# Kernel optimization log

Hardware: AMD Instinct MI355X
Metric: run time of the kernel (lower is better)

Reference implementation:

```python
import jax, jax.numpy as jnp
import numpy as np

N_NODES = 100000
N_EDGES = 1600000
N_GRAPHS = 256
DIMS = [128, 128, 128, 128]  # gcn_layers_dim -> 3 GCNConv layers


def setup_inputs() -> dict:
    key = jax.random.key(0)
    ks = jax.random.split(key, 12)
    inp = {
        "x": jax.random.normal(ks[0], (N_NODES, DIMS[0]), jnp.float32),
        "edge_index": jax.random.randint(ks[1], (2, N_EDGES), 0, N_NODES),
        "edge_weight": jax.random.uniform(ks[2], (N_EDGES,), jnp.float32),
        "batch": jnp.sort(jax.random.randint(ks[3], (N_NODES,), 0, N_GRAPHS)),
    }
    for i in range(3):
        fan_in = DIMS[i]
        scale = 1.0 / np.sqrt(fan_in)
        inp[f"W{i+1}"] = jax.random.uniform(ks[4 + 2 * i], (DIMS[i], DIMS[i + 1]),
                                             jnp.float32, -scale, scale)
        inp[f"b{i+1}"] = jax.random.uniform(ks[5 + 2 * i], (DIMS[i + 1],),
                                             jnp.float32, -scale, scale)
    return inp


def reference(x, edge_index, edge_weight, batch, W1, b1, W2, b2, W3, b3):
    n = x.shape[0]
    # PyG GCNConv: add self-loops with weight 1, symmetric normalization.
    loop = jnp.arange(n)
    row = jnp.concatenate([edge_index[0], loop])  # source nodes
    col = jnp.concatenate([edge_index[1], loop])  # target nodes (aggregation index)
    w = jnp.concatenate([edge_weight, jnp.ones((n,), x.dtype)])
    deg = jax.ops.segment_sum(w, col, num_segments=n)
    dinv = jnp.where(deg > 0, jax.lax.rsqrt(deg), jnp.zeros_like(deg))
    norm = dinv[row] * w * dinv[col]  # [E+N]

    # global_mean_pool setup
    counts = jax.ops.segment_sum(jnp.ones((n,), x.dtype), batch,
                                 num_segments=N_GRAPHS)
    counts = jnp.maximum(counts, 1.0)[:, None]

    def gcn_conv(h, W, b):
        hl = h @ W                      # linear projection first (PyG order)
        msg = hl[row] * norm[:, None]   # gather + edge scaling
        out = jax.ops.segment_sum(msg, col, num_segments=n)  # scatter-add
        return out + b

    embeddings = []
    h = x
    for W, b in ((W1, b1), (W2, b2), (W3, b3)):
        h = gcn_conv(h, W, b)
        h = jax.nn.relu(h)              # relu_layers_index = [0,1,2]
        emb = jax.ops.segment_sum(h, batch, num_segments=N_GRAPHS) / counts
        embeddings.append(emb)          # gep = global_mean_pool
    return tuple(embeddings)
```

## Files before the change

kernel.cpp:

```cpp
#include <hip/hip_runtime.h>


typedef short short8 __attribute__((ext_vector_type(8)));
typedef float f32x4  __attribute__((ext_vector_type(4)));

__device__ inline unsigned pack_bf16x2(float a, float b) {
    unsigned ua = __float_as_uint(a);
    ua = (ua + 0x7FFFu + ((ua >> 16) & 1u)) >> 16;
    unsigned ub = __float_as_uint(b);
    ub = (ub + 0x7FFFu + ((ub >> 16) & 1u)) >> 16;
    return ua | (ub << 16);
}
__device__ inline ushort bf16_1(float a) {
    unsigned ua = __float_as_uint(a);
    return (ushort)((ua + 0x7FFFu + ((ua >> 16) & 1u)) >> 16);
}
__device__ inline float bf_lo(unsigned u) { return __uint_as_float(u << 16); }
__device__ inline float bf_hi(unsigned u) { return __uint_as_float(u & 0xFFFF0000u); }

__global__ void k_zero(int* __restrict__ cnt, int N) {
    int i = blockIdx.x * blockDim.x + threadIdx.x;
    if (i < N) cnt[i] = 0;
}

__global__ void k_phase1(const int* __restrict__ ei, int* __restrict__ cnt,
                         int* __restrict__ epos, int E) {
    int e = blockIdx.x * blockDim.x + threadIdx.x;
    if (e >= E) return;
    int c = ei[E + e];
    epos[e] = atomicAdd(&cnt[c], 1);
}

__global__ __launch_bounds__(1024) void k_scan1(const int* __restrict__ cnt,
                                                int* __restrict__ pre,
                                                int* __restrict__ bsum, int n) {
    __shared__ int wsum[16];
    int t = threadIdx.x, lane = t & 63, w = t >> 6;
    int i = blockIdx.x * 1024 + t;
    int v = (i < n) ? cnt[i] : 0;
    int x = v;
#pragma unroll
    for (int off = 1; off < 64; off <<= 1) {
        int y = __shfl_up(x, off, 64);
        if (lane >= off) x += y;
    }
    if (lane == 63) wsum[w] = x;
    __syncthreads();
    int woff = 0, tot = 0;
#pragma unroll
    for (int q = 0; q < 16; q++) { int s = wsum[q]; if (q < w) woff += s; tot += s; }
    if (i < n) pre[i] = woff + x - v;
    if (t == 0) bsum[blockIdx.x] = tot;
}

__global__ __launch_bounds__(128) void k_scan2(int* __restrict__ bsum, int nb,
                                               int* __restrict__ ptrv, int n) {
    __shared__ int ws[2];
    int t = threadIdx.x, lane = t & 63, w = t >> 6;
    int v = (t < nb) ? bsum[t] : 0;
    int x = v;
#pragma unroll
    for (int off = 1; off < 64; off <<= 1) {
        int y = __shfl_up(x, off, 64);
        if (lane >= off) x += y;
    }
    if (lane == 63) ws[w] = x;
    __syncthreads();
    int woff = (w == 1) ? ws[0] : 0;
    int tot = ws[0] + ws[1];
    if (t < nb) bsum[t] = woff + x - v;
    if (t == 0) ptrv[n] = tot;
}

__global__ __launch_bounds__(1024) void k_scan3(const int* __restrict__ pre,
                                                const int* __restrict__ bsum,
                                                int* __restrict__ ptrv, int n) {
    int i = blockIdx.x * 1024 + threadIdx.x;
    if (i >= n) return;
    ptrv[i] = pre[i] + bsum[blockIdx.x];
}

__global__ void k_scatter(const int* __restrict__ ei, const float* __restrict__ ew,
                          const int* __restrict__ ptrv, const int* __restrict__ epos,
                          int2* __restrict__ csr, int E) {
    int e = blockIdx.x * blockDim.x + threadIdx.x;
    if (e >= E) return;
    int r = ei[e];
    int c = ei[E + e];
    int2 v; v.x = r; v.y = __float_as_int(ew[e]);
    csr[ptrv[c] + epos[e]] = v;
}

__global__ void k_degdinv(const int2* __restrict__ csr, const int* __restrict__ ptrv,
                          float* __restrict__ dinv, int N) {
    int i = blockIdx.x * blockDim.x + threadIdx.x;
    if (i >= N) return;
    float s = 1.0f;
    int e1 = ptrv[i + 1];
    for (int j = ptrv[i]; j < e1; j++) s += __int_as_float(csr[j].y);
    dinv[i] = (s > 0.f) ? rsqrtf(s) : 0.f;
}

__global__ void k_norm(int2* __restrict__ csr, const int* __restrict__ ptrv,
                       const float* __restrict__ dinv, int N) {
    int i = blockIdx.x * blockDim.x + threadIdx.x;
    if (i >= N) return;
    float dc = dinv[i];
    int e1 = ptrv[i + 1];
    for (int j = ptrv[i]; j < e1; j++) {
        int2 m = csr[j];
        m.y = __float_as_int(dinv[m.x] * __int_as_float(m.y) * dc);
        csr[j] = m;
    }
}

__global__ void k_bounds(const int* __restrict__ batch, int* __restrict__ gb,
                         int N, int G) {
    int t = blockIdx.x * blockDim.x + threadIdx.x;
    if (t > G) return;
    int lo = 0, hi = N;
    while (lo < hi) { int mid = (lo + hi) >> 1; if (batch[mid] < t) lo = mid + 1; else hi = mid; }
    gb[t] = lo;
}

__global__ void k_wprep(const float* __restrict__ W0, const float* __restrict__ W1,
                        const float* __restrict__ W2, ushort* __restrict__ WbT) {
    int l = blockIdx.y;
    const float* W = (l == 0) ? W0 : ((l == 1) ? W1 : W2);
    int id = blockIdx.x * 256 + threadIdx.x;
    int n = id & 127, k = id >> 7;
    WbT[l * 16384 + n * 128 + k] = bf16_1(W[k * 128 + n]);
}

__global__ __launch_bounds__(256) void k_gemm_f32(const float* __restrict__ Hin,
                                                  const float* __restrict__ W,
                                                  unsigned* __restrict__ O, int M) {
    __shared__ float sH[64 * 128];
    int t = threadIdx.x;
    int rbase = blockIdx.x * 64;
    int nrows = M - rbase; if (nrows > 64) nrows = 64;
    float4* sH4 = (float4*)sH;
    int nf = nrows * 32;
    const float4* H4 = (const float4*)Hin + (size_t)rbase * 32;
#pragma unroll
    for (int i = 0; i < 8; i++) {
        int idx = t + i * 256;
        float4 v = make_float4(0.f, 0.f, 0.f, 0.f);
        if (idx < nf) v = H4[idx];
        sH4[idx] = v;
    }
    __syncthreads();
    int jc = t & 31;
    int rg = t >> 5;
    const float4* W4 = (const float4*)W;
    float4 acc[8];
#pragma unroll
    for (int r = 0; r < 8; r++) acc[r] = make_float4(0.f, 0.f, 0.f, 0.f);
    const float* hrow = &sH[rg * 8 * 128];
#pragma unroll 4
    for (int k = 0; k < 128; k++) {
        float4 wv = W4[k * 32 + jc];
#pragma unroll
        for (int r = 0; r < 8; r++) {
            float hv = hrow[r * 128 + k];
            acc[r].x += hv * wv.x;
            acc[r].y += hv * wv.y;
            acc[r].z += hv * wv.z;
            acc[r].w += hv * wv.w;
        }
    }
    uint2* O2 = (uint2*)O;
#pragma unroll
    for (int r = 0; r < 8; r++) {
        int row = rbase + rg * 8 + r;
        if (row < M) {
            uint2 pv;
            pv.x = pack_bf16x2(acc[r].x, acc[r].y);
            pv.y = pack_bf16x2(acc[r].z, acc[r].w);
            O2[(size_t)row * 32 + jc] = pv;
        }
    }
}

__global__ __launch_bounds__(256) void k_gemm_mfma(const unsigned* __restrict__ Hb,
                                                   const ushort* __restrict__ WbT,
                                                   unsigned* __restrict__ O, int M) {
    __shared__ unsigned sOut[4 * 32 * 64];
    int lane = threadIdx.x & 63;
    int wv = threadIdx.x >> 6;
    int quad = lane >> 4;
    int mrow = lane & 15;
    int m0 = blockIdx.x * 128 + wv * 32;
    int r0 = m0 + mrow;
    int r1 = r0 + 16;
    int r0c = r0 < M ? r0 : M - 1;
    int r1c = r1 < M ? r1 : M - 1;

    short8 a0[4], a1[4];
#pragma unroll
    for (int s = 0; s < 4; s++) {
        a0[s] = *(const short8*)(Hb + (size_t)r0c * 64 + s * 16 + quad * 4);
        a1[s] = *(const short8*)(Hb + (size_t)r1c * 64 + s * 16 + quad * 4);
    }
    f32x4 acc0[8], acc1[8];
#pragma unroll
    for (int t = 0; t < 8; t++) {
        acc0[t] = (f32x4){0.f, 0.f, 0.f, 0.f};
        acc1[t] = (f32x4){0.f, 0.f, 0.f, 0.f};
    }
#pragma unroll
    for (int s = 0; s < 4; s++) {
#pragma unroll
        for (int t = 0; t < 8; t++) {
            short8 b = *(const short8*)(WbT + (t * 16 + mrow) * 128 + s * 32 + quad * 8);
            acc0[t] = __builtin_amdgcn_mfma_f32_16x16x32_bf16(a0[s], b, acc0[t], 0, 0, 0);
            acc1[t] = __builtin_amdgcn_mfma_f32_16x16x32_bf16(a1[s], b, acc1[t], 0, 0, 0);
        }
    }
    ushort* so = (ushort*)(sOut + wv * 32 * 64);
#pragma unroll
    for (int t = 0; t < 8; t++) {
#pragma unroll
        for (int r = 0; r < 4; r++) {
            int lr = quad * 4 + r;
            int c = t * 16 + mrow;
            so[lr * 128 + c] = bf16_1(acc0[t][r]);
            so[(lr + 16) * 128 + c] = bf16_1(acc1[t][r]);
        }
    }
    __syncthreads();
    const unsigned* si = sOut + wv * 32 * 64;
#pragma unroll 8
    for (int r = 0; r < 32; r++) {
        int row = m0 + r;
        if (row < M) O[(size_t)row * 64 + lane] = si[r * 64 + lane];
    }
}

__global__ __launch_bounds__(256) void k_agg(const unsigned* __restrict__ HL,
                                             const int* __restrict__ ptr,
                                             const int2* __restrict__ csr,
                                             const float* __restrict__ dinv,
                                             const float* __restrict__ bias,
                                             unsigned* __restrict__ Hout, int M) {
    __shared__ int2 sM[4 * 64];
    int node = (int)((blockIdx.x * blockDim.x + threadIdx.x) >> 6);
    if (node >= M) return;
    int lane = threadIdx.x & 63;
    int2* mbase = &sM[(threadIdx.x >> 6) * 64];
    int e0 = ptr[node], e1 = ptr[node + 1];
    int deg = e1 - e0;
    int nb = deg < 64 ? deg : 64;
    if (lane < nb) mbase[lane] = csr[e0 + lane];
    float di = dinv[node];
    float sn = di * di;
    unsigned u0 = HL[(size_t)node * 64 + lane];
    float ax = sn * bf_lo(u0), ay = sn * bf_hi(u0);
    int j = 0;
    for (; j + 8 <= nb; j += 8) {
        int2 m[8];
        unsigned u[8];
#pragma unroll
        for (int q = 0; q < 8; q++) m[q] = mbase[j + q];
#pragma unroll
        for (int q = 0; q < 8; q++) u[q] = HL[(size_t)m[q].x * 64 + lane];
#pragma unroll
        for (int q = 0; q < 8; q++) {
            float nv = __int_as_float(m[q].y);
            ax += nv * bf_lo(u[q]);
            ay += nv * bf_hi(u[q]);
        }
    }
    for (; j < nb; j++) {
        int2 m = mbase[j];
        unsigned u = HL[(size_t)m.x * 64 + lane];
        float nv = __int_as_float(m.y);
        ax += nv * bf_lo(u);
        ay += nv * bf_hi(u);
    }
    for (int e = e0 + 64; e < e1; e++) {
        int2 m = csr[e];
        unsigned u = HL[(size_t)m.x * 64 + lane];
        float nv = __int_as_float(m.y);
        ax += nv * bf_lo(u);
        ay += nv * bf_hi(u);
    }
    float2 bv = ((const float2*)bias)[lane];
    float rx = fmaxf(ax + bv.x, 0.f);
    float ry = fmaxf(ay + bv.y, 0.f);
    Hout[(size_t)node * 64 + lane] = pack_bf16x2(rx, ry);
}

__global__ __launch_bounds__(256) void k_pool(const unsigned* __restrict__ HB,
                                              const int* __restrict__ gb,
                                              float* __restrict__ outp) {
    __shared__ float part[4][128];
    int g = blockIdx.x;
    int lane = threadIdx.x & 63, w = threadIdx.x >> 6;
    int s = gb[g], e = gb[g + 1];
    float ax = 0.f, ay = 0.f;
    for (int i = s + w; i < e; i += 4) {
        unsigned u = HB[(size_t)i * 64 + lane];
        ax += bf_lo(u); ay += bf_hi(u);
    }
    part[w][lane * 2] = ax;
    part[w][lane * 2 + 1] = ay;
    __syncthreads();
    if (threadIdx.x < 128) {
        float sum = part[0][threadIdx.x] + part[1][threadIdx.x]
                  + part[2][threadIdx.x] + part[3][threadIdx.x];
        float c = (float)(e - s);
        outp[g * 128 + threadIdx.x] = sum / fmaxf(c, 1.0f);
    }
}

extern "C" void kernel_launch(void* const* d_in, const int* in_sizes, int n_in,
                              void* d_out, int out_size, void* d_ws, size_t ws_size,
                              hipStream_t stream) {
    const float* x     = (const float*)d_in[0];
    const int*   ei    = (const int*)d_in[1];
    const float* ew    = (const float*)d_in[2];
    const int*   batch = (const int*)d_in[3];
    const float* Wt[3] = {(const float*)d_in[4], (const float*)d_in[6], (const float*)d_in[8]};
    const float* bt[3] = {(const float*)d_in[5], (const float*)d_in[7], (const float*)d_in[9]};
    float* out = (float*)d_out;

    const int D = 128;
    const int N = in_sizes[0] / D;
    const int E = in_sizes[2];
    const int G = out_size / (3 * D);

    char* p = (char*)d_ws;
    auto alloc = [&](size_t bytes) {
        void* r = (void*)p;
        p += (bytes + 255) & ~(size_t)255;
        return r;
    };
    int*      cnt    = (int*)alloc((size_t)N * 4);
    int*      ptr    = (int*)alloc((size_t)(N + 1) * 4);
    int*      pre    = (int*)alloc((size_t)N * 4);
    int*      bsum   = (int*)alloc((size_t)128 * 4);
    int*      gb     = (int*)alloc((size_t)(G + 1) * 4);
    float*    dinv   = (float*)alloc((size_t)N * 4);
    ushort*   WbT    = (ushort*)alloc((size_t)3 * 16384 * 2);
    int2*     csr    = (int2*)alloc((size_t)E * 8);
    unsigned* bufHL  = (unsigned*)alloc((size_t)N * 64 * 4);
    unsigned* bufH   = (unsigned*)alloc((size_t)N * 64 * 4);
    int*      epos   = (int*)bufH;

    int nb = (N + 1023) / 1024;

    k_zero<<<(N + 255) / 256, 256, 0, stream>>>(cnt, N);
    k_phase1<<<(E + 255) / 256, 256, 0, stream>>>(ei, cnt, epos, E);
    k_bounds<<<1, 512, 0, stream>>>(batch, gb, N, G);
    k_wprep<<<dim3(64, 3), 256, 0, stream>>>(Wt[0], Wt[1], Wt[2], WbT);
    k_scan1<<<nb, 1024, 0, stream>>>(cnt, pre, bsum, N);
    k_scan2<<<1, 128, 0, stream>>>(bsum, nb, ptr, N);
    k_scan3<<<nb, 1024, 0, stream>>>(pre, bsum, ptr, N);
    k_scatter<<<(E + 255) / 256, 256, 0, stream>>>(ei, ew, ptr, epos, csr, E);
    k_degdinv<<<(N + 255) / 256, 256, 0, stream>>>(csr, ptr, dinv, N);
    k_norm<<<(N + 255) / 256, 256, 0, stream>>>(csr, ptr, dinv, N);

    for (int l = 0; l < 3; l++) {
        if (l == 0)
            k_gemm_f32<<<(N + 63) / 64, 256, 0, stream>>>(x, Wt[0], bufHL, N);
        else
            k_gemm_mfma<<<(N + 127) / 128, 256, 0, stream>>>(bufH, WbT + (size_t)l * 16384,
                                                             bufHL, N);
        k_agg<<<(N + 3) / 4, 256, 0, stream>>>(bufHL, ptr, csr, dinv, bt[l], bufH, N);
        k_pool<<<G, 256, 0, stream>>>(bufH, gb, out + (size_t)l * G * D);
    }
}
```

Baseline: 616.7 us.

## Use MFMA for first-layer GEMM and split edges across half-waves in aggregation

The first layer's fp32 SIMT GEMM is replaced by the bf16 MFMA GEMM, templated to read fp32 input and convert it to bf16 in registers. This lowers compute cost but rounds the input features to bf16. The aggregation kernel now has each half-wave handle alternate edges, with each lane loading 8 bytes (4 features) per edge. The halves are combined with a cross-half shuffle. This aims to double the concurrent gathers per wave and use wider loads, at the cost of half the lanes idling on the store.

```diff
diff --git a/kernel.cpp b/kernel.cpp
--- a/kernel.cpp
+++ b/kernel.cpp
@@ -132,57 +132,8 @@
     WbT[l * 16384 + n * 128 + k] = bf16_1(W[k * 128 + n]);
 }
 
-__global__ __launch_bounds__(256) void k_gemm_f32(const float* __restrict__ Hin,
-                                                  const float* __restrict__ W,
-                                                  unsigned* __restrict__ O, int M) {
-    __shared__ float sH[64 * 128];
-    int t = threadIdx.x;
-    int rbase = blockIdx.x * 64;
-    int nrows = M - rbase; if (nrows > 64) nrows = 64;
-    float4* sH4 = (float4*)sH;
-    int nf = nrows * 32;
-    const float4* H4 = (const float4*)Hin + (size_t)rbase * 32;
-#pragma unroll
-    for (int i = 0; i < 8; i++) {
-        int idx = t + i * 256;
-        float4 v = make_float4(0.f, 0.f, 0.f, 0.f);
-        if (idx < nf) v = H4[idx];
-        sH4[idx] = v;
-    }
-    __syncthreads();
-    int jc = t & 31;
-    int rg = t >> 5;
-    const float4* W4 = (const float4*)W;
-    float4 acc[8];
-#pragma unroll
-    for (int r = 0; r < 8; r++) acc[r] = make_float4(0.f, 0.f, 0.f, 0.f);
-    const float* hrow = &sH[rg * 8 * 128];
-#pragma unroll 4
-    for (int k = 0; k < 128; k++) {
-        float4 wv = W4[k * 32 + jc];
-#pragma unroll
-        for (int r = 0; r < 8; r++) {
-            float hv = hrow[r * 128 + k];
-            acc[r].x += hv * wv.x;
-            acc[r].y += hv * wv.y;
-            acc[r].z += hv * wv.z;
-            acc[r].w += hv * wv.w;
-        }
-    }
-    uint2* O2 = (uint2*)O;
-#pragma unroll
-    for (int r = 0; r < 8; r++) {
-        int row = rbase + rg * 8 + r;
-        if (row < M) {
-            uint2 pv;
-            pv.x = pack_bf16x2(acc[r].x, acc[r].y);
-            pv.y = pack_bf16x2(acc[r].z, acc[r].w);
-            O2[(size_t)row * 32 + jc] = pv;
-        }
-    }
-}
-
-__global__ __launch_bounds__(256) void k_gemm_mfma(const unsigned* __restrict__ Hb,
+template <bool F32IN>
+__global__ __launch_bounds__(256) void k_gemm_mfma(const void* __restrict__ Hin,
                                                    const ushort* __restrict__ WbT,
                                                    unsigned* __restrict__ O, int M) {
     __shared__ unsigned sOut[4 * 32 * 64];
@@ -197,10 +148,28 @@
     int r1c = r1 < M ? r1 : M - 1;
 
     short8 a0[4], a1[4];
-#pragma unroll
-    for (int s = 0; s < 4; s++) {
-        a0[s] = *(const short8*)(Hb + (size_t)r0c * 64 + s * 16 + quad * 4);
-        a1[s] = *(const short8*)(Hb + (size_t)r1c * 64 + s * 16 + quad * 4);
+    if (F32IN) {
+        const float* Hf = (const float*)Hin;
+#pragma unroll
+        for (int s = 0; s < 4; s++) {
+            const float4* p0 = (const float4*)(Hf + (size_t)r0c * 128 + s * 32 + quad * 8);
+            const float4* p1 = (const float4*)(Hf + (size_t)r1c * 128 + s * 32 + quad * 8);
+            float4 f0 = p0[0], f1 = p0[1];
+            float4 g0 = p1[0], g1 = p1[1];
+            union { short8 s8; unsigned u[4]; } t0, t1;
+            t0.u[0] = pack_bf16x2(f0.x, f0.y); t0.u[1] = pack_bf16x2(f0.z, f0.w);
+            t0.u[2] = pack_bf16x2(f1.x, f1.y); t0.u[3] = pack_bf16x2(f1.z, f1.w);
+            t1.u[0] = pack_bf16x2(g0.x, g0.y); t1.u[1] = pack_bf16x2(g0.z, g0.w);
+            t1.u[2] = pack_bf16x2(g1.x, g1.y); t1.u[3] = pack_bf16x2(g1.z, g1.w);
+            a0[s] = t0.s8; a1[s] = t1.s8;
+        }
+    } else {
+        const unsigned* Hb = (const unsigned*)Hin;
+#pragma unroll
+        for (int s = 0; s < 4; s++) {
+            a0[s] = *(const short8*)(Hb + (size_t)r0c * 64 + s * 16 + quad * 4);
+            a1[s] = *(const short8*)(Hb + (size_t)r1c * 64 + s * 16 + quad * 4);
+        }
     }
     f32x4 acc0[8], acc1[8];
 #pragma unroll
@@ -247,48 +216,62 @@
     int node = (int)((blockIdx.x * blockDim.x + threadIdx.x) >> 6);
     if (node >= M) return;
     int lane = threadIdx.x & 63;
+    int half = lane >> 5;
+    int q = lane & 31;
     int2* mbase = &sM[(threadIdx.x >> 6) * 64];
     int e0 = ptr[node], e1 = ptr[node + 1];
     int deg = e1 - e0;
-    int nb = deg < 64 ? deg : 64;
-    if (lane < nb) mbase[lane] = csr[e0 + lane];
+    int nbv = deg < 64 ? deg : 64;
+    if (lane < nbv) mbase[lane] = csr[e0 + lane];
+    const uint2* HL2 = (const uint2*)HL;
     float di = dinv[node];
-    float sn = di * di;
-    unsigned u0 = HL[(size_t)node * 64 + lane];
-    float ax = sn * bf_lo(u0), ay = sn * bf_hi(u0);
-    int j = 0;
-    for (; j + 8 <= nb; j += 8) {
-        int2 m[8];
-        unsigned u[8];
-#pragma unroll
-        for (int q = 0; q < 8; q++) m[q] = mbase[j + q];
-#pragma unroll
-        for (int q = 0; q < 8; q++) u[q] = HL[(size_t)m[q].x * 64 + lane];
-#pragma unroll
-        for (int q = 0; q < 8; q++) {
-            float nv = __int_as_float(m[q].y);
-            ax += nv * bf_lo(u[q]);
-            ay += nv * bf_hi(u[q]);
-        }
-    }
-    for (; j < nb; j++) {
+    float sn = (half == 0) ? di * di : 0.f;
+    uint2 us = HL2[(size_t)node * 32 + q];
+    float a0 = sn * bf_lo(us.x), a1 = sn * bf_hi(us.x);
+    float a2 = sn * bf_lo(us.y), a3 = sn * bf_hi(us.y);
+    int j = half;
+    for (; j + 8 <= nbv; j += 8) {
+        int2 m[4]; uint2 u[4];
+#pragma unroll
+        for (int t = 0; t < 4; t++) m[t] = mbase[j + 2 * t];
+#pragma unroll
+        for (int t = 0; t < 4; t++) u[t] = HL2[(size_t)m[t].x * 32 + q];
+#pragma unroll
+        for (int t = 0; t < 4; t++) {
+            float nv = __int_as_float(m[t].y);
+            a0 += nv * bf_lo(u[t].x); a1 += nv * bf_hi(u[t].x);
+            a2 += nv * bf_lo(u[t].y); a3 += nv * bf_hi(u[t].y);
+        }
+    }
+    for (; j < nbv; j += 2) {
         int2 m = mbase[j];
-        unsigned u = HL[(size_t)m.x * 64 + lane];
+        uint2 u = HL2[(size_t)m.x * 32 + q];
         float nv = __int_as_float(m.y);
-        ax += nv * bf_lo(u);
-        ay += nv * bf_hi(u);
-    }
-    for (int e = e0 + 64; e < e1; e++) {
+        a0 += nv * bf_lo(u.x); a1 += nv * bf_hi(u.x);
+        a2 += nv * bf_lo(u.y); a3 += nv * bf_hi(u.y);
+    }
+    for (int e = e0 + 64 + half; e < e1; e += 2) {
         int2 m = csr[e];
-        unsigned u = HL[(size_t)m.x * 64 + lane];
+        uint2 u = HL2[(size_t)m.x * 32 + q];
         float nv = __int_as_float(m.y);
-        ax += nv * bf_lo(u);
-        ay += nv * bf_hi(u);
-    }
-    float2 bv = ((const float2*)bias)[lane];
-    float rx = fmaxf(ax + bv.x, 0.f);
-    float ry = fmaxf(ay + bv.y, 0.f);
-    Hout[(size_t)node * 64 + lane] = pack_bf16x2(rx, ry);
+        a0 += nv * bf_lo(u.x); a1 += nv * bf_hi(u.x);
+        a2 += nv * bf_lo(u.y); a3 += nv * bf_hi(u.y);
+    }
+    a0 += __shfl_xor(a0, 32, 64);
+    a1 += __shfl_xor(a1, 32, 64);
+    a2 += __shfl_xor(a2, 32, 64);
+    a3 += __shfl_xor(a3, 32, 64);
+    float4 bv = ((const float4*)bias)[q];
+    float r0 = fmaxf(a0 + bv.x, 0.f);
+    float r1 = fmaxf(a1 + bv.y, 0.f);
+    float r2 = fmaxf(a2 + bv.z, 0.f);
+    float r3 = fmaxf(a3 + bv.w, 0.f);
+    if (half == 0) {
+        uint2 pv;
+        pv.x = pack_bf16x2(r0, r1);
+        pv.y = pack_bf16x2(r2, r3);
+        ((uint2*)(Hout + (size_t)node * 64))[q] = pv;
+    }
 }
 
 __global__ __launch_bounds__(256) void k_pool(const unsigned* __restrict__ HB,
@@ -363,10 +346,10 @@
 
     for (int l = 0; l < 3; l++) {
         if (l == 0)
-            k_gemm_f32<<<(N + 63) / 64, 256, 0, stream>>>(x, Wt[0], bufHL, N);
+            k_gemm_mfma<true><<<(N + 127) / 128, 256, 0, stream>>>(x, WbT, bufHL, N);
         else
-            k_gemm_mfma<<<(N + 127) / 128, 256, 0, stream>>>(bufH, WbT + (size_t)l * 16384,
-                                                             bufHL, N);
+            k_gemm_mfma<false><<<(N + 127) / 128, 256, 0, stream>>>(bufH, WbT + (size_t)l * 16384,
+                                                                    bufHL, N);
         k_agg<<<(N + 3) / 4, 256, 0, stream>>>(bufHL, ptr, csr, dinv, bt[l], bufH, N);
         k_pool<<<G, 256, 0, stream>>>(bufH, gb, out + (size_t)l * G * D);
     }
```

After: 600.7 us. -2.6%, faster.
